# Kernel optimization log

Hardware: AMD Instinct MI355X
Metric: run time of the kernel (lower is better)

## Reference

```python
import jax, jax.numpy as jnp
import numpy as np

D = 2048          # input_size
B_NECK = 512      # bottleneck_size
NUM_LANGS = 16
ZETA = 1.1
GAMMA = -0.1
LN_EPS = 1e-5


def setup_inputs() -> dict:
    key = jax.random.key(0)
    ks = jax.random.split(key, 8)
    x = jax.random.normal(ks[0], (8, 2048, D), dtype=jnp.float32)
    # xavier_uniform for linear weights
    lim_d = float(np.sqrt(6.0 / (D + B_NECK)))
    down_w = jax.random.uniform(ks[1], (B_NECK, D), minval=-lim_d, maxval=lim_d, dtype=jnp.float32)
    up_w = jax.random.uniform(ks[2], (D, B_NECK), minval=-lim_d, maxval=lim_d, dtype=jnp.float32)
    down_b = jnp.zeros((B_NECK,), dtype=jnp.float32)
    up_b = jnp.zeros((D,), dtype=jnp.float32)
    ln_g = jnp.ones((D,), dtype=jnp.float32)
    ln_b = jnp.zeros((D,), dtype=jnp.float32)
    down_loga = 0.01 * jax.random.normal(ks[3], (NUM_LANGS, D), dtype=jnp.float32)
    up_loga = 0.01 * jax.random.normal(ks[4], (NUM_LANGS, B_NECK), dtype=jnp.float32)
    return {"x": x, "down_w": down_w, "down_b": down_b, "up_w": up_w,
            "up_b": up_b, "ln_g": ln_g, "ln_b": ln_b,
            "down_loga": down_loga, "up_loga": up_loga, "lang_id": 3}


def _det_mask(loga_row):
    # eval-mode L0 gate: hardtanh(sigmoid(loga)*(zeta-gamma)+gamma, 0, 1)
    return jnp.clip(jax.nn.sigmoid(loga_row) * (ZETA - GAMMA) + GAMMA, 0.0, 1.0)


def reference(x, down_w, down_b, up_w, up_b, ln_g, ln_b, down_loga, up_loga, lang_id):
    shortcut = x
    # LayerNorm over last dim
    mu = jnp.mean(x, axis=-1, keepdims=True)
    var = jnp.mean(jnp.square(x - mu), axis=-1, keepdims=True)
    h = (x - mu) * jax.lax.rsqrt(var + LN_EPS) * ln_g + ln_b
    # down projection with per-input-feature gate (mask scales weight columns)
    dmask = _det_mask(down_loga[lang_id])            # [D]
    h = jnp.einsum('bsd,kd->bsk', h * dmask, down_w) + down_b  # [B,S,B_NECK]
    h = jax.nn.relu(h)
    # up projection with per-bottleneck gate
    umask = _det_mask(up_loga[lang_id])              # [B_NECK]
    h = jnp.einsum('bsk,dk->bsd', h * umask, up_w) + up_b       # [B,S,D]
    return h + shortcut
```

## Files before the change

### kernel.cpp

```cpp
#include <hip/hip_runtime.h>
#include <cstdint>
#include <cstddef>

typedef unsigned short u16;
typedef __attribute__((ext_vector_type(4))) float f32x4;
typedef __attribute__((ext_vector_type(8))) short bf16x8;

#define LN_EPS 1e-5f
#define WAITV(n) asm volatile("s_waitcnt vmcnt(" #n ")" ::: "memory")
#define LGKM0    asm volatile("s_waitcnt lgkmcnt(0)" ::: "memory")
#define BAR()    do { __builtin_amdgcn_s_barrier(); asm volatile("" ::: "memory"); } while (0)

__device__ __forceinline__ u16 f2bf(float f) {
  unsigned int u = __float_as_uint(f);
  u += 0x7FFFu + ((u >> 16) & 1u);
  return (u16)(u >> 16);
}

__device__ __forceinline__ float l0gate(float loga) {
  float s = 1.0f / (1.0f + expf(-loga));
  float v = s * 1.2f - 0.1f;
  return fminf(fmaxf(v, 0.0f), 1.0f);
}

__device__ __forceinline__ void llds16(u16* lds, const u16* g) {
  __builtin_amdgcn_global_load_lds(
      (const __attribute__((address_space(1))) unsigned int*)g,
      (__attribute__((address_space(3))) unsigned int*)lds, 16, 0, 0);
}

__global__ __launch_bounds__(256) void prep_weights(
    const float* __restrict__ dw, const float* __restrict__ uw,
    const float* __restrict__ dloga, const float* __restrict__ uloga,
    const int* __restrict__ lang,
    u16* __restrict__ dwb, u16* __restrict__ uwb) {
  const int lid = lang[0];
  const unsigned i = blockIdx.x * 256u + threadIdx.x;
  dwb[i] = f2bf(dw[i] * l0gate(dloga[lid * 2048 + (i & 2047u)]));
  uwb[i] = f2bf(uw[i] * l0gate(uloga[lid * 512 + (i & 511u)]));
}

__global__ __launch_bounds__(256) void ln_kernel(
    const float* __restrict__ x, const float* __restrict__ g,
    const float* __restrict__ b, u16* __restrict__ h1) {
  const int row = blockIdx.x;
  const int tid = threadIdx.x;
  const float4* xr = (const float4*)(x + (size_t)row * 2048);
  float4 v0 = xr[tid * 2 + 0];
  float4 v1 = xr[tid * 2 + 1];
  float s = v0.x + v0.y + v0.z + v0.w + v1.x + v1.y + v1.z + v1.w;
  float q = v0.x * v0.x + v0.y * v0.y + v0.z * v0.z + v0.w * v0.w +
            v1.x * v1.x + v1.y * v1.y + v1.z * v1.z + v1.w * v1.w;
#pragma unroll
  for (int off = 32; off > 0; off >>= 1) {
    s += __shfl_down(s, off, 64);
    q += __shfl_down(q, off, 64);
  }
  __shared__ float ss[4], sq[4], sstat[2];
  const int wave = tid >> 6, lane = tid & 63;
  if (lane == 0) { ss[wave] = s; sq[wave] = q; }
  __syncthreads();
  if (tid == 0) {
    float S = ss[0] + ss[1] + ss[2] + ss[3];
    float Q = sq[0] + sq[1] + sq[2] + sq[3];
    float mu = S * (1.0f / 2048.0f);
    float var = Q * (1.0f / 2048.0f) - mu * mu;
    sstat[0] = mu;
    sstat[1] = rsqrtf(var + LN_EPS);
  }
  __syncthreads();
  const float mu = sstat[0], rs = sstat[1];
  const float4* g4 = (const float4*)g;
  const float4* b4 = (const float4*)b;
  float4 ga = g4[tid * 2], gb = g4[tid * 2 + 1];
  float4 ba = b4[tid * 2], bb = b4[tid * 2 + 1];
  union { u16 us[8]; uint4 u; } p;
  p.us[0] = f2bf((v0.x - mu) * rs * ga.x + ba.x);
  p.us[1] = f2bf((v0.y - mu) * rs * ga.y + ba.y);
  p.us[2] = f2bf((v0.z - mu) * rs * ga.z + ba.z);
  p.us[3] = f2bf((v0.w - mu) * rs * ga.w + ba.w);
  p.us[4] = f2bf((v1.x - mu) * rs * gb.x + bb.x);
  p.us[5] = f2bf((v1.y - mu) * rs * gb.y + bb.y);
  p.us[6] = f2bf((v1.z - mu) * rs * gb.z + bb.z);
  p.us[7] = f2bf((v1.w - mu) * rs * gb.w + bb.w);
  ((uint4*)(h1 + (size_t)row * 2048))[tid] = p.u;
}

__global__ __launch_bounds__(256) void gemm1(
    const u16* __restrict__ A, const u16* __restrict__ Bw,
    int M, int K, int NX,
    const float* __restrict__ bias,
    u16* __restrict__ outp) {
  const int N = 512;
  __shared__ __align__(16) char smem[81920];
  u16* Sg = (u16*)smem;
  float* Cs = (float*)smem;

  const int tid = threadIdx.x;
  const int wave = tid >> 6, lane = tid & 63;
  const int wr = (wave >> 1) * 64, wc = (wave & 1) * 64;
  const int lrow = lane & 15, lk = lane >> 4;

  const int nwg = gridDim.x;
  const int wg = (blockIdx.x & 7) * (nwg >> 3) + (blockIdx.x >> 3);
  const int bx = wg % NX, by = wg / NX;
  const size_t m0 = (size_t)by * 128, n0 = (size_t)bx * 128;

  f32x4 acc[4][4] = {};

  const int srow = lane >> 3;
  const int sslot = ((lane & 7) ^ ((lane >> 3) & 7)) * 8;
  auto SA = [&](int buf, int k0) {
#pragma unroll
    for (int c = 0; c < 4; ++c) {
      const int seg = c * 4 + wave;
      llds16(Sg + buf * 8192 + seg * 512,
             A + (m0 + seg * 8 + srow) * (size_t)K + (k0 + sslot));
    }
  };
  auto SB = [&](int buf, int k0) {
#pragma unroll
    for (int c = 0; c < 4; ++c) {
      const int seg = c * 4 + wave;
      llds16(Sg + 24576 + buf * 8192 + seg * 512,
             Bw + (n0 + seg * 8 + srow) * (size_t)K + (k0 + sslot));
    }
  };

  const int NT = K >> 6;
  SB(0, 0); SA(0, 0); SA(1, 64);

  for (int t = 0; t < NT; ++t) {
    if (t + 1 < NT) SB((t + 1) & 1, (t + 1) << 6);
    if (t + 2 < NT) SA((t + 2) % 3, (t + 2) << 6);
    if (t < NT - 2)       WAITV(12);
    else if (t == NT - 2) WAITV(8);
    else                  WAITV(0);
    BAR();

    const u16* Ab = Sg + (t % 3) * 8192;
    const u16* Bb = Sg + 24576 + (t & 1) * 8192;
#pragma unroll
    for (int ks = 0; ks < 2; ++ks) {
      bf16x8 af[4], bfr[4];
#pragma unroll
      for (int m = 0; m < 4; ++m)
        af[m] = *(const bf16x8*)&Ab[(wr + m * 16 + lrow) * 64 +
                                    ((unsigned)((ks * 4 + lk) ^ (lane & 7))) * 8];
#pragma unroll
      for (int n = 0; n < 4; ++n)
        bfr[n] = *(const bf16x8*)&Bb[(wc + n * 16 + lrow) * 64 +
                                     ((unsigned)((ks * 4 + lk) ^ (lane & 7))) * 8];
      __builtin_amdgcn_s_setprio(1);
#pragma unroll
      for (int m = 0; m < 4; ++m)
#pragma unroll
        for (int n = 0; n < 4; ++n)
          acc[m][n] = __builtin_amdgcn_mfma_f32_16x16x32_bf16(af[m], bfr[n],
                                                              acc[m][n], 0, 0, 0);
      __builtin_amdgcn_s_setprio(0);
    }
    LGKM0;
    BAR();
  }

#pragma unroll
  for (int n = 0; n < 4; ++n) {
    const int c = wc + n * 16 + lrow;
    const float bv = bias[n0 + c];
#pragma unroll
    for (int m = 0; m < 4; ++m) {
#pragma unroll
      for (int r = 0; r < 4; ++r) {
        const int row = wr + m * 16 + lk * 4 + r;
        Cs[row * 128 + ((c + ((row >> 2) << 3)) & 127)] = acc[m][n][r] + bv;
      }
    }
  }
  LGKM0;
  BAR();

#pragma unroll
  for (int j = 0; j < 8; ++j) {
    const int flat = tid * 8 + j * 2048;
    const int row = flat >> 7, c = flat & 127;
    const int cp = (c + ((row >> 2) << 3)) & 127;
    const f32x4 c0 = *(const f32x4*)&Cs[row * 128 + cp];
    const f32x4 c1 = *(const f32x4*)&Cs[row * 128 + cp + 4];
    union { u16 us[8]; uint4 u; } p;
    p.us[0] = f2bf(fmaxf(c0[0], 0.0f)); p.us[1] = f2bf(fmaxf(c0[1], 0.0f));
    p.us[2] = f2bf(fmaxf(c0[2], 0.0f)); p.us[3] = f2bf(fmaxf(c0[3], 0.0f));
    p.us[4] = f2bf(fmaxf(c1[0], 0.0f)); p.us[5] = f2bf(fmaxf(c1[1], 0.0f));
    p.us[6] = f2bf(fmaxf(c1[2], 0.0f)); p.us[7] = f2bf(fmaxf(c1[3], 0.0f));
    *(uint4*)&outp[(m0 + row) * (size_t)N + n0 + c] = p.u;
  }
}

__global__ __launch_bounds__(256) void gemm2(
    const u16* __restrict__ A, const u16* __restrict__ Bw,
    int M, const float* __restrict__ bias,
    const float* __restrict__ resid, float* __restrict__ outp) {
  const int K = 512, N = 2048;
  __shared__ __align__(16) char smem[81920];
  u16* Sg = (u16*)smem;
  float* Cs = (float*)smem;

  const int tid = threadIdx.x;
  const int wave = tid >> 6, lane = tid & 63;
  const int wr = (wave >> 1) * 64, wc = (wave & 1) * 64;
  const int lrow = lane & 15, lk = lane >> 4;

  const int nwg = gridDim.x;
  const int wg = (blockIdx.x & 7) * (nwg >> 3) + (blockIdx.x >> 3);
  const int bx = wg & 15, by = wg >> 4;
  const size_t m0 = (size_t)by * 128, n0 = (size_t)bx * 128;

  f32x4 acc[4][4] = {};

  const int srow = lane >> 3;
  const int sslot = ((lane & 7) ^ ((lane >> 3) & 7)) * 8;
  auto SA = [&](int buf, int k0) {
#pragma unroll
    for (int c = 0; c < 4; ++c) {
      const int seg = c * 4 + wave;
      llds16(Sg + buf * 8192 + seg * 512,
             A + (m0 + seg * 8 + srow) * (size_t)K + (k0 + sslot));
    }
  };
  auto SB = [&](int buf, int k0) {
#pragma unroll
    for (int c = 0; c < 4; ++c) {
      const int seg = c * 4 + wave;
      llds16(Sg + 24576 + buf * 8192 + seg * 512,
             Bw + (n0 + seg * 8 + srow) * (size_t)K + (k0 + sslot));
    }
  };

  f32x4 rsd[16];
  auto RSD = [&](int j) {
    const int flat = tid * 4 + j * 1024;
    const int row = flat >> 7, c = flat & 127;
    rsd[j] = *(const f32x4*)&resid[(m0 + row) * (size_t)N + n0 + c];
  };

  SB(0, 0); SA(0, 0); SA(1, 64);

#pragma unroll
  for (int t = 0; t < 8; ++t) {
    if (t + 1 < 8) SB((t + 1) & 1, (t + 1) * 64);
    if (t + 2 < 8) SA((t + 2) % 3, (t + 2) * 64);
    if (t < 7) { RSD(2 * t); RSD(2 * t + 1); }
    else       { RSD(14); RSD(15); }
    if (t == 0)      WAITV(14);
    else if (t <= 5) WAITV(16);
    else if (t == 6) WAITV(12);
    else             WAITV(4);
    BAR();

    const u16* Ab = Sg + (t % 3) * 8192;
    const u16* Bb = Sg + 24576 + (t & 1) * 8192;
#pragma unroll
    for (int ks = 0; ks < 2; ++ks) {
      bf16x8 af[4], bfr[4];
#pragma unroll
      for (int m = 0; m < 4; ++m)
        af[m] = *(const bf16x8*)&Ab[(wr + m * 16 + lrow) * 64 +
                                    ((unsigned)((ks * 4 + lk) ^ (lane & 7))) * 8];
#pragma unroll
      for (int n = 0; n < 4; ++n)
        bfr[n] = *(const bf16x8*)&Bb[(wc + n * 16 + lrow) * 64 +
                                     ((unsigned)((ks * 4 + lk) ^ (lane & 7))) * 8];
      __builtin_amdgcn_s_setprio(1);
#pragma unroll
      for (int m = 0; m < 4; ++m)
#pragma unroll
        for (int n = 0; n < 4; ++n)
          acc[m][n] = __builtin_amdgcn_mfma_f32_16x16x32_bf16(af[m], bfr[n],
                                                              acc[m][n], 0, 0, 0);
      __builtin_amdgcn_s_setprio(0);
    }
    LGKM0;
    BAR();
  }

#pragma unroll
  for (int n = 0; n < 4; ++n) {
    const int c = wc + n * 16 + lrow;
    const float bv = bias[n0 + c];
#pragma unroll
    for (int m = 0; m < 4; ++m) {
#pragma unroll
      for (int r = 0; r < 4; ++r) {
        const int row = wr + m * 16 + lk * 4 + r;
        Cs[row * 128 + ((c + ((row >> 2) << 3)) & 127)] = acc[m][n][r] + bv;
      }
    }
  }
  LGKM0;
  BAR();

#pragma unroll
  for (int j = 0; j < 16; ++j) {
    const int flat = tid * 4 + j * 1024;
    const int row = flat >> 7, c = flat & 127;
    const f32x4 cc = *(const f32x4*)&Cs[row * 128 + ((c + ((row >> 2) << 3)) & 127)];
    f32x4 o;
    o[0] = cc[0] + rsd[j][0]; o[1] = cc[1] + rsd[j][1];
    o[2] = cc[2] + rsd[j][2]; o[3] = cc[3] + rsd[j][3];
    *(f32x4*)&outp[(m0 + row) * (size_t)N + n0 + c] = o;
  }
}

extern "C" void kernel_launch(void* const* d_in, const int* in_sizes, int n_in,
                              void* d_out, int out_size, void* d_ws, size_t ws_size,
                              hipStream_t stream) {
  const float* x         = (const float*)d_in[0];
  const float* down_w    = (const float*)d_in[1];
  const float* down_b    = (const float*)d_in[2];
  const float* up_w      = (const float*)d_in[3];
  const float* up_b      = (const float*)d_in[4];
  const float* ln_g      = (const float*)d_in[5];
  const float* ln_b      = (const float*)d_in[6];
  const float* down_loga = (const float*)d_in[7];
  const float* up_loga   = (const float*)d_in[8];
  const int*   lang      = (const int*)d_in[9];

  const int D = 2048, BNK = 512;
  const int M = in_sizes[0] / D;

  char* ws = (char*)d_ws;
  u16* h1  = (u16*)ws;
  u16* h2  = (u16*)(ws + (size_t)M * D * 2);
  u16* dwb = (u16*)(ws + (size_t)M * D * 2 + (size_t)M * BNK * 2);
  u16* uwb = dwb + (size_t)BNK * D;

  prep_weights<<<(BNK * D) / 256, 256, 0, stream>>>(down_w, up_w, down_loga,
                                                    up_loga, lang, dwb, uwb);
  ln_kernel<<<M, 256, 0, stream>>>(x, ln_g, ln_b, h1);
  gemm1<<<(M / 128) * (BNK / 128), 256, 0, stream>>>(h1, dwb, M, D, BNK / 128,
                                                     down_b, h2);
  gemm2<<<(M / 128) * (D / 128), 256, 0, stream>>>(h2, uwb, M, up_b, x,
                                                   (float*)d_out);
}
```

Measured before the change: 148.4 us.

## Fold LayerNorm into GEMM1 epilogue and read bf16 residual in GEMM2

```diff
diff --git a/kernel.cpp b/kernel.cpp
--- a/kernel.cpp
+++ b/kernel.cpp
@@ -5,6 +5,7 @@
 typedef unsigned short u16;
 typedef __attribute__((ext_vector_type(4))) float f32x4;
 typedef __attribute__((ext_vector_type(8))) short bf16x8;
+typedef __attribute__((ext_vector_type(4))) short bf16x4;
 
 #define LN_EPS 1e-5f
 #define WAITV(n) asm volatile("s_waitcnt vmcnt(" #n ")" ::: "memory")
@@ -17,6 +18,10 @@
   return (u16)(u >> 16);
 }
 
+__device__ __forceinline__ float bf2f(short b) {
+  return __uint_as_float(((unsigned)(unsigned short)b) << 16);
+}
+
 __device__ __forceinline__ float l0gate(float loga) {
   float s = 1.0f / (1.0f + expf(-loga));
   float v = s * 1.2f - 0.1f;
@@ -32,17 +37,38 @@
 __global__ __launch_bounds__(256) void prep_weights(
     const float* __restrict__ dw, const float* __restrict__ uw,
     const float* __restrict__ dloga, const float* __restrict__ uloga,
-    const int* __restrict__ lang,
+    const int* __restrict__ lang, const float* __restrict__ g,
     u16* __restrict__ dwb, u16* __restrict__ uwb) {
   const int lid = lang[0];
   const unsigned i = blockIdx.x * 256u + threadIdx.x;
-  dwb[i] = f2bf(dw[i] * l0gate(dloga[lid * 2048 + (i & 2047u)]));
+  dwb[i] = f2bf(dw[i] * l0gate(dloga[lid * 2048 + (i & 2047u)]) * g[i & 2047u]);
   uwb[i] = f2bf(uw[i] * l0gate(uloga[lid * 512 + (i & 511u)]));
 }
 
-__global__ __launch_bounds__(256) void ln_kernel(
-    const float* __restrict__ x, const float* __restrict__ g,
-    const float* __restrict__ b, u16* __restrict__ h1) {
+__global__ __launch_bounds__(256) void prep_uv(
+    const float* __restrict__ dw, const float* __restrict__ dloga,
+    const int* __restrict__ lang, const float* __restrict__ g,
+    const float* __restrict__ lnb, const float* __restrict__ down_b,
+    float* __restrict__ u, float* __restrict__ wv) {
+  const int lid = lang[0];
+  const int n = blockIdx.x * 4 + (threadIdx.x >> 6);
+  const int lane = threadIdx.x & 63;
+  float su = 0.0f, sv = 0.0f;
+  for (int d = lane; d < 2048; d += 64) {
+    const float w = dw[n * 2048 + d] * l0gate(dloga[lid * 2048 + d]);
+    su += w * g[d];
+    sv += w * lnb[d];
+  }
+#pragma unroll
+  for (int off = 32; off > 0; off >>= 1) {
+    su += __shfl_down(su, off, 64);
+    sv += __shfl_down(sv, off, 64);
+  }
+  if (lane == 0) { u[n] = su; wv[n] = sv + down_b[n]; }
+}
+
+__global__ __launch_bounds__(256) void stats_cast(
+    const float* __restrict__ x, u16* __restrict__ xb, float* __restrict__ ST) {
   const int row = blockIdx.x;
   const int tid = threadIdx.x;
   const float4* xr = (const float4*)(x + (size_t)row * 2048);
@@ -56,7 +82,7 @@
     s += __shfl_down(s, off, 64);
     q += __shfl_down(q, off, 64);
   }
-  __shared__ float ss[4], sq[4], sstat[2];
+  __shared__ float ss[4], sq[4];
   const int wave = tid >> 6, lane = tid & 63;
   if (lane == 0) { ss[wave] = s; sq[wave] = q; }
   __syncthreads();
@@ -65,31 +91,22 @@
     float Q = sq[0] + sq[1] + sq[2] + sq[3];
     float mu = S * (1.0f / 2048.0f);
     float var = Q * (1.0f / 2048.0f) - mu * mu;
-    sstat[0] = mu;
-    sstat[1] = rsqrtf(var + LN_EPS);
-  }
-  __syncthreads();
-  const float mu = sstat[0], rs = sstat[1];
-  const float4* g4 = (const float4*)g;
-  const float4* b4 = (const float4*)b;
-  float4 ga = g4[tid * 2], gb = g4[tid * 2 + 1];
-  float4 ba = b4[tid * 2], bb = b4[tid * 2 + 1];
+    ST[2 * row] = mu;
+    ST[2 * row + 1] = rsqrtf(var + LN_EPS);
+  }
   union { u16 us[8]; uint4 u; } p;
-  p.us[0] = f2bf((v0.x - mu) * rs * ga.x + ba.x);
-  p.us[1] = f2bf((v0.y - mu) * rs * ga.y + ba.y);
-  p.us[2] = f2bf((v0.z - mu) * rs * ga.z + ba.z);
-  p.us[3] = f2bf((v0.w - mu) * rs * ga.w + ba.w);
-  p.us[4] = f2bf((v1.x - mu) * rs * gb.x + bb.x);
-  p.us[5] = f2bf((v1.y - mu) * rs * gb.y + bb.y);
-  p.us[6] = f2bf((v1.z - mu) * rs * gb.z + bb.z);
-  p.us[7] = f2bf((v1.w - mu) * rs * gb.w + bb.w);
-  ((uint4*)(h1 + (size_t)row * 2048))[tid] = p.u;
+  p.us[0] = f2bf(v0.x); p.us[1] = f2bf(v0.y);
+  p.us[2] = f2bf(v0.z); p.us[3] = f2bf(v0.w);
+  p.us[4] = f2bf(v1.x); p.us[5] = f2bf(v1.y);
+  p.us[6] = f2bf(v1.z); p.us[7] = f2bf(v1.w);
+  ((uint4*)(xb + (size_t)row * 2048))[tid] = p.u;
 }
 
 __global__ __launch_bounds__(256) void gemm1(
     const u16* __restrict__ A, const u16* __restrict__ Bw,
     int M, int K, int NX,
-    const float* __restrict__ bias,
+    const float* __restrict__ uu, const float* __restrict__ wvv,
+    const float* __restrict__ ST,
     u16* __restrict__ outp) {
   const int N = 512;
   __shared__ __align__(16) char smem[81920];
@@ -164,16 +181,24 @@
     BAR();
   }
 
+  float ucol[4], wcol[4];
 #pragma unroll
   for (int n = 0; n < 4; ++n) {
     const int c = wc + n * 16 + lrow;
-    const float bv = bias[n0 + c];
-#pragma unroll
-    for (int m = 0; m < 4; ++m) {
-#pragma unroll
-      for (int r = 0; r < 4; ++r) {
-        const int row = wr + m * 16 + lk * 4 + r;
-        Cs[row * 128 + ((c + ((row >> 2) << 3)) & 127)] = acc[m][n][r] + bv;
+    ucol[n] = uu[n0 + c];
+    wcol[n] = wvv[n0 + c];
+  }
+#pragma unroll
+  for (int m = 0; m < 4; ++m) {
+#pragma unroll
+    for (int r = 0; r < 4; ++r) {
+      const int row = wr + m * 16 + lk * 4 + r;
+      const float2 ms = *(const float2*)&ST[2 * (m0 + row)];
+#pragma unroll
+      for (int n = 0; n < 4; ++n) {
+        const int c = wc + n * 16 + lrow;
+        const float val = ms.y * (acc[m][n][r] - ms.x * ucol[n]) + wcol[n];
+        Cs[row * 128 + ((c + ((row >> 2) << 3)) & 127)] = val;
       }
     }
   }
@@ -199,7 +224,7 @@
 __global__ __launch_bounds__(256) void gemm2(
     const u16* __restrict__ A, const u16* __restrict__ Bw,
     int M, const float* __restrict__ bias,
-    const float* __restrict__ resid, float* __restrict__ outp) {
+    const u16* __restrict__ xb, float* __restrict__ outp) {
   const int K = 512, N = 2048;
   __shared__ __align__(16) char smem[81920];
   u16* Sg = (u16*)smem;
@@ -236,11 +261,11 @@
     }
   };
 
-  f32x4 rsd[16];
+  bf16x4 rsdb[16];
   auto RSD = [&](int j) {
     const int flat = tid * 4 + j * 1024;
     const int row = flat >> 7, c = flat & 127;
-    rsd[j] = *(const f32x4*)&resid[(m0 + row) * (size_t)N + n0 + c];
+    rsdb[j] = *(const bf16x4*)&xb[(m0 + row) * (size_t)N + n0 + c];
   };
 
   SB(0, 0); SA(0, 0); SA(1, 64);
@@ -305,8 +330,8 @@
     const int row = flat >> 7, c = flat & 127;
     const f32x4 cc = *(const f32x4*)&Cs[row * 128 + ((c + ((row >> 2) << 3)) & 127)];
     f32x4 o;
-    o[0] = cc[0] + rsd[j][0]; o[1] = cc[1] + rsd[j][1];
-    o[2] = cc[2] + rsd[j][2]; o[3] = cc[3] + rsd[j][3];
+#pragma unroll
+    for (int e = 0; e < 4; ++e) o[e] = cc[e] + bf2f(rsdb[j][e]);
     *(f32x4*)&outp[(m0 + row) * (size_t)N + n0 + c] = o;
   }
 }
@@ -329,16 +354,21 @@
   const int M = in_sizes[0] / D;
 
   char* ws = (char*)d_ws;
-  u16* h1  = (u16*)ws;
-  u16* h2  = (u16*)(ws + (size_t)M * D * 2);
-  u16* dwb = (u16*)(ws + (size_t)M * D * 2 + (size_t)M * BNK * 2);
-  u16* uwb = dwb + (size_t)BNK * D;
+  u16*   xb  = (u16*)ws;
+  u16*   h2  = (u16*)(ws + (size_t)M * D * 2);
+  u16*   dwb = (u16*)(ws + (size_t)M * D * 2 + (size_t)M * BNK * 2);
+  u16*   uwb = dwb + (size_t)BNK * D;
+  float* u_  = (float*)(uwb + (size_t)D * BNK);
+  float* wv_ = u_ + BNK;
+  float* ST  = wv_ + BNK;
 
   prep_weights<<<(BNK * D) / 256, 256, 0, stream>>>(down_w, up_w, down_loga,
-                                                    up_loga, lang, dwb, uwb);
-  ln_kernel<<<M, 256, 0, stream>>>(x, ln_g, ln_b, h1);
-  gemm1<<<(M / 128) * (BNK / 128), 256, 0, stream>>>(h1, dwb, M, D, BNK / 128,
-                                                     down_b, h2);
-  gemm2<<<(M / 128) * (D / 128), 256, 0, stream>>>(h2, uwb, M, up_b, x,
+                                                    up_loga, lang, ln_g, dwb, uwb);
+  prep_uv<<<BNK / 4, 256, 0, stream>>>(down_w, down_loga, lang, ln_g, ln_b,
+                                       down_b, u_, wv_);
+  stats_cast<<<M, 256, 0, stream>>>(x, xb, ST);
+  gemm1<<<(M / 128) * (BNK / 128), 256, 0, stream>>>(xb, dwb, M, D, BNK / 128,
+                                                     u_, wv_, ST, h2);
+  gemm2<<<(M / 128) * (D / 128), 256, 0, stream>>>(h2, uwb, M, up_b, xb,
                                                    (float*)d_out);
 }
```

New measurement: 155.0 us. 4.5% more time.
